# Kernel tuning notes

Measured on AMD Instinct MI355X. Metric: run time of the kernel, lower is better.

## Reference

```python
import jax, jax.numpy as jnp
import numpy as np

N = 512          # N_ROIs (nodes)
E = N * N        # number of edges
V = 6            # number of views (edge_attr dim)
DIMS = [(1, 36), (36, 24), (24, 5)]  # (in, out) per NNConv layer


def _nnconv(x, edge_attr, src, dst, We, be, root, bias, cin, cout):
    # edge MLP: Linear + ReLU -> per-edge weight matrix [E, cin, cout]
    w = jax.nn.relu(edge_attr @ We + be).reshape(-1, cin, cout)
    msg = jnp.einsum('ei,eio->eo', x[src], w)              # gather + per-edge matmul
    s = jax.ops.segment_sum(msg, dst, num_segments=N)      # scatter-sum
    cnt = jax.ops.segment_sum(jnp.ones((msg.shape[0], 1), x.dtype), dst, num_segments=N)
    agg = s / jnp.maximum(cnt, 1.0)                        # mean aggregation
    return agg + x @ root + bias                           # root weight + bias (PyG NNConv)


def setup_inputs() -> dict:
    key = jax.random.key(0)
    ks = jax.random.split(key, 16)
    x = jnp.ones((N, 1), jnp.float32)
    edge_attr = jax.random.uniform(ks[0], (E, V), jnp.float32)
    edge_index = jax.random.randint(ks[1], (2, E), 0, N, dtype=jnp.int32)
    inp = {'x': x, 'edge_attr': edge_attr, 'edge_index': edge_index}
    for l, (cin, cout) in enumerate(DIMS, start=1):
        k = jax.random.split(ks[1 + l], 4)
        inp[f'We{l}'] = jax.random.normal(k[0], (V, cin * cout), jnp.float32) / np.sqrt(V)
        inp[f'be{l}'] = jnp.zeros((cin * cout,), jnp.float32)
        inp[f'root{l}'] = jax.random.normal(k[1], (cin, cout), jnp.float32) / np.sqrt(cin)
        inp[f'b{l}'] = jnp.zeros((cout,), jnp.float32)
    return inp


def reference(x, edge_attr, edge_index,
              We1, be1, root1, b1,
              We2, be2, root2, b2,
              We3, be3, root3, b3):
    src, dst = edge_index[0], edge_index[1]
    h = jax.nn.relu(_nnconv(x, edge_attr, src, dst, We1, be1, root1, b1, *DIMS[0]))
    h = jax.nn.relu(_nnconv(h, edge_attr, src, dst, We2, be2, root2, b2, *DIMS[1]))
    h = jax.nn.relu(_nnconv(h, edge_attr, src, dst, We3, be3, root3, b3, *DIMS[2]))
    # pairwise CBT: sum_k |h_i,k - h_j,k|  ->  [N, N]
    cbt = jnp.sum(jnp.abs(h[:, None, :] - h[None, :, :]), axis=2)
    return cbt
```

## Files before the change

### kernel.cpp

```cpp
#include <hip/hip_runtime.h>
#include <hip/hip_bf16.h>
#include <hip/hip_fp16.h>

#define N_NODES 512
#define N_EDGES (512 * 512)
#define NBLK 256
#define EPB (N_EDGES / NBLK)
#define PADLEN 768

typedef __attribute__((ext_vector_type(8))) __bf16 bf16x8;
typedef __attribute__((ext_vector_type(16))) float f32x16;

static __device__ inline unsigned bf16rne(float f) {
    union { float f; unsigned u; } c;
    c.f = f;
    unsigned u = c.u;
    u += 0x7FFFu + ((u >> 16) & 1u);
    return u >> 16;
}
static __device__ inline float bf2f(unsigned h) {
    union { unsigned u; float f; } c;
    c.u = h << 16;
    return c.f;
}

__global__ __launch_bounds__(256) void count_kernel(const int* __restrict__ dst,
                                                    int* __restrict__ bcnt) {
    __shared__ int h[N_NODES];
    int tid = threadIdx.x;
    int b = blockIdx.x;
    h[tid] = 0;
    h[tid + 256] = 0;
    __syncthreads();
#pragma unroll
    for (int k = 0; k < EPB / 256; k++)
        atomicAdd(&h[dst[b * EPB + k * 256 + tid]], 1);
    __syncthreads();
    bcnt[b * N_NODES + tid] = h[tid];
    bcnt[b * N_NODES + tid + 256] = h[tid + 256];
}

__global__ __launch_bounds__(512) void scan_kernel(const int* __restrict__ bcnt,
                                                   int* __restrict__ offs,
                                                   int* __restrict__ base) {
    __shared__ int buf[N_NODES];
    int t = threadIdx.x;
    int sum = 0;
#pragma unroll 16
    for (int b = 0; b < NBLK; b++) sum += bcnt[b * N_NODES + t];
    buf[t] = sum;
    __syncthreads();
    for (int d = 1; d < N_NODES; d <<= 1) {
        int add = (t >= d) ? buf[t - d] : 0;
        __syncthreads();
        buf[t] += add;
        __syncthreads();
    }
    offs[t + 1] = buf[t];
    if (t == 0) offs[0] = 0;
    int run = buf[t] - sum;
#pragma unroll 16
    for (int b = 0; b < NBLK; b++) {
        base[b * N_NODES + t] = run;
        run += bcnt[b * N_NODES + t];
    }
}

__global__ __launch_bounds__(256) void scatter_kernel(const int* __restrict__ src,
                                                      const int* __restrict__ dst,
                                                      const float* __restrict__ ea,
                                                      const int* __restrict__ base,
                                                      const int* __restrict__ offs,
                                                      int4* __restrict__ edp,
                                                      int* __restrict__ srcp) {
    __shared__ int lcur[N_NODES];
    __shared__ int loff[N_NODES];
    int tid = threadIdx.x;
    int b = blockIdx.x;
    lcur[tid] = base[b * N_NODES + tid];
    lcur[tid + 256] = base[b * N_NODES + tid + 256];
    loff[tid] = offs[tid];
    loff[tid + 256] = offs[tid + 256];
    __syncthreads();
    const unsigned ONE = 0x3F80u;
#pragma unroll
    for (int k = 0; k < EPB / 256; k++) {
        int e = b * EPB + k * 256 + tid;
        const float* a = ea + (size_t)e * 6;
        unsigned e0 = bf16rne(a[0]), e1 = bf16rne(a[1]), e2 = bf16rne(a[2]);
        unsigned e3 = bf16rne(a[3]), e4 = bf16rne(a[4]), e5 = bf16rne(a[5]);
        int dv = dst[e], sv = src[e];
        int p = atomicAdd(&lcur[dv], 1);
        int rank = p - loff[dv];
        size_t pi = (size_t)dv * PADLEN + rank;
        int4 r0, r1;
        r0.x = (int)((e1 << 16) | e0);
        r0.y = (int)((e3 << 16) | e2);
        r0.z = (int)((e5 << 16) | e4);
        r0.w = (int)((e0 << 16) | ONE);
        r1.x = (int)((e2 << 16) | e1);
        r1.y = (int)((e4 << 16) | e3);
        r1.z = (int)((ONE << 16) | e5);
        r1.w = 0;
        edp[pi * 2] = r0;
        edp[pi * 2 + 1] = r1;
        srcp[pi] = sv;
    }
}

__global__ __launch_bounds__(256) void wprep_kernel(const float* __restrict__ We,
                                                    const float* __restrict__ be,
                                                    int Jr, int total,
                                                    int4* __restrict__ wtg) {
    int idx = blockIdx.x * 256 + threadIdx.x;
    if (idx >= total) return;
    int t = idx >> 6, lane = idx & 63, col = lane & 31, hi = lane >> 5;
    int j = t * 32 + col;
    unsigned h[8] = {0, 0, 0, 0, 0, 0, 0, 0};
    if (j < Jr) {
        unsigned wh[6];
        float wl[6];
        for (int v = 0; v < 6; v++) {
            float wv = We[v * Jr + j];
            wh[v] = bf16rne(wv);
            wl[v] = wv - bf2f(wh[v]);
        }
        float bev = be[j];
        unsigned bh = bf16rne(bev);
        float bl = bev - bf2f(bh);
        if (hi == 0) {
            for (int v = 0; v < 6; v++) h[v] = wh[v];
            h[6] = bh;
            h[7] = bf16rne(wl[0]);
        } else {
            for (int v = 1; v < 6; v++) h[v - 1] = bf16rne(wl[v]);
            h[5] = bf16rne(bl);
            h[6] = 0;
            h[7] = 0;
        }
    }
    int4 r;
    r.x = (int)((h[1] << 16) | h[0]);
    r.y = (int)((h[3] << 16) | h[2]);
    r.z = (int)((h[5] << 16) | h[4]);
    r.w = (int)((h[7] << 16) | h[6]);
    wtg[idx] = r;
}

template <int CIN, int COUT, int TILES, int SLOTS>
__global__ __launch_bounds__(512, 4) void nnconv_mfma(
    const float* __restrict__ hprev,
    const int4* __restrict__ edp,
    const int* __restrict__ srcp,
    const int* __restrict__ offs,
    const int4* __restrict__ wtg,
    const float* __restrict__ root,
    const float* __restrict__ bias,
    float* __restrict__ hout)
{
    __shared__ __half xs[N_NODES * CIN];
    __shared__ int4 wl[TILES * 64];
    __shared__ float lagg[COUT];

    const int tid = threadIdx.x;
    const int n = blockIdx.x;

    for (int k = tid; k < N_NODES * CIN; k += 512) xs[k] = __float2half(hprev[k]);
    for (int k = tid; k < TILES * 64; k += 512) wl[k] = wtg[k];
    if (tid < COUT) lagg[tid] = 0.f;
    __syncthreads();

    const int w = tid >> 6, lane = tid & 63;
    const int col = lane & 31, hi = lane >> 5;
    const char* xsp = (const char*)xs;
    const char* wlp = (const char*)wl + (hi * 32 + col) * 16;

    f32x16 zc;
#pragma unroll
    for (int q = 0; q < 16; q++) zc[q] = 0.f;

    float ao[SLOTS];
#pragma unroll
    for (int s = 0; s < SLOTS; s++) ao[s] = 0.f;

    const int nb = n * PADLEN + w * 96;

    for (int c = 0; c < 3; c++) {
        const int cb = nb + c * 32;
        bf16x8 af = *(const bf16x8*)((const char*)edp + (size_t)(cb + col) * 32 + hi * 16);
        int xb[16];
#pragma unroll
        for (int qq = 0; qq < 4; qq++) {
            int4 sv = *(const int4*)(srcp + cb + qq * 8 + hi * 4);
            xb[qq * 4 + 0] = sv.x * (CIN * 2);
            xb[qq * 4 + 1] = sv.y * (CIN * 2);
            xb[qq * 4 + 2] = sv.z * (CIN * 2);
            xb[qq * 4 + 3] = sv.w * (CIN * 2);
        }
        const char* wq = wlp;
        int jb = col;
#pragma unroll 1
        for (int tt = 0; tt < TILES / SLOTS; tt++) {
#pragma unroll
            for (int s = 0; s < SLOTS; s++) {
                bf16x8 bf = *(const bf16x8*)(wq + s * 1024);
                f32x16 ct = __builtin_amdgcn_mfma_f32_32x32x16_bf16(af, bf, zc, 0, 0, 0);
                int j = jb + s * 32;
                int i = j / COUT;
                if (i > CIN - 1) i = CIN - 1;
                int i2 = i * 2;
#pragma unroll
                for (int r = 0; r < 16; r++) {
                    float xv = __half2float(*(const __half*)(xsp + xb[r] + i2));
                    ao[s] = fmaf(fmaxf(ct[r], 0.f), xv, ao[s]);
                }
            }
            wq += SLOTS * 1024;
            jb += SLOTS * 32;
        }
    }

#pragma unroll
    for (int s = 0; s < SLOTS; s++) {
        int o = (s * 32 + col) % COUT;
        atomicAdd(&lagg[o], ao[s]);
    }
    __syncthreads();

    if (tid < COUT) {
        int cnt = offs[n + 1] - offs[n];
        float v = lagg[tid] / fmaxf((float)cnt, 1.f);
#pragma unroll
        for (int i = 0; i < CIN; i++)
            v = fmaf(hprev[n * CIN + i], root[i * COUT + tid], v);
        hout[n * COUT + tid] = fmaxf(v + bias[tid], 0.f);
    }
}

__global__ __launch_bounds__(256) void cbt_kernel(const float* __restrict__ h3,
                                                  float* __restrict__ out) {
    __shared__ float lh[N_NODES * 5];
    int tid = threadIdx.x;
    for (int idx = tid; idx < N_NODES * 5; idx += 256) lh[idx] = h3[idx];
    __syncthreads();
    int i = blockIdx.x;
    float hi[5];
#pragma unroll
    for (int k = 0; k < 5; k++) hi[k] = lh[i * 5 + k];
    for (int j = tid; j < N_NODES; j += 256) {
        float sacc = 0.f;
#pragma unroll
        for (int k = 0; k < 5; k++) sacc += fabsf(hi[k] - lh[j * 5 + k]);
        out[i * N_NODES + j] = sacc;
    }
}

extern "C" void kernel_launch(void* const* d_in, const int* in_sizes, int n_in,
                              void* d_out, int out_size, void* d_ws, size_t ws_size,
                              hipStream_t stream) {
    const float* x = (const float*)d_in[0];
    const float* edge_attr = (const float*)d_in[1];
    const int* edge_index = (const int*)d_in[2];
    const float* We1 = (const float*)d_in[3];
    const float* be1 = (const float*)d_in[4];
    const float* root1 = (const float*)d_in[5];
    const float* b1 = (const float*)d_in[6];
    const float* We2 = (const float*)d_in[7];
    const float* be2 = (const float*)d_in[8];
    const float* root2 = (const float*)d_in[9];
    const float* b2 = (const float*)d_in[10];
    const float* We3 = (const float*)d_in[11];
    const float* be3 = (const float*)d_in[12];
    const float* root3 = (const float*)d_in[13];
    const float* b3 = (const float*)d_in[14];

    const int E = N_EDGES;
    const int* src = edge_index;
    const int* dst = edge_index + E;

    char* ws = (char*)d_ws;
    int* offs = (int*)(ws + 0);
    int* bcnt = (int*)(ws + 4096);
    int* base = (int*)(ws + 528384);
    int4* edp = (int4*)(ws + 1052672);
    int* srcp = (int*)(ws + 13635584);
    int4* wtg1 = (int4*)(ws + 15208448);
    int4* wtg2 = (int4*)(ws + 15210496);
    int4* wtg3 = (int4*)(ws + 15238144);
    float* h1 = (float*)(ws + 15242240);
    float* h2 = (float*)(ws + 15315968);
    float* h3 = (float*)(ws + 15365120);

    hipMemsetAsync(edp, 0, (size_t)N_NODES * PADLEN * 32 + (size_t)N_NODES * PADLEN * 4, stream);

    count_kernel<<<NBLK, 256, 0, stream>>>(dst, bcnt);
    scan_kernel<<<1, 512, 0, stream>>>(bcnt, offs, base);
    scatter_kernel<<<NBLK, 256, 0, stream>>>(src, dst, edge_attr, base, offs, edp, srcp);

    wprep_kernel<<<1, 256, 0, stream>>>(We1, be1, 36, 2 * 64, wtg1);
    wprep_kernel<<<7, 256, 0, stream>>>(We2, be2, 864, 27 * 64, wtg2);
    wprep_kernel<<<1, 256, 0, stream>>>(We3, be3, 120, 4 * 64, wtg3);

    nnconv_mfma<1, 36, 2, 2><<<N_NODES, 512, 0, stream>>>(x, edp, srcp, offs, wtg1, root1, b1, h1);
    nnconv_mfma<36, 24, 27, 3><<<N_NODES, 512, 0, stream>>>(h1, edp, srcp, offs, wtg2, root2, b2, h2);
    nnconv_mfma<24, 5, 4, 4><<<N_NODES, 512, 0, stream>>>(h2, edp, srcp, offs, wtg3, root3, b3, h3);

    cbt_kernel<<<N_NODES, 256, 0, stream>>>(h3, (float*)d_out);
}
```

Measured before the change: 220.2 us.

## Swap MFMA operand roles and pad weight layout to per-input-channel tiles

Swaps the MFMA operands so edges lie along the column dimension and weight outputs along the rows. Weights are padded so each tile row maps to a single input channel, which lets each lane hold its source node's features in registers. Loaded once per edge chunk from a padded half-precision copy emitted by the previous layer, they replace per-row LDS gathers and the full LDS staging of hprev. Reduction moves to cross-lane shuffles before the LDS atomics. In exchange, padding adds more MFMA tiles (36 vs 27 for layer 2) and more accumulator registers.

```diff
diff --git a/kernel.cpp b/kernel.cpp
--- a/kernel.cpp
+++ b/kernel.cpp
@@ -22,6 +22,9 @@
     union { unsigned u; float f; } c;
     c.u = h << 16;
     return c.f;
+}
+static __device__ __forceinline__ int i4c(const int4& v, int c) {
+    return c == 0 ? v.x : (c == 1 ? v.y : (c == 2 ? v.z : v.w));
 }
 
 __global__ __launch_bounds__(256) void count_kernel(const int* __restrict__ dst,
@@ -42,9 +45,12 @@
 
 __global__ __launch_bounds__(512) void scan_kernel(const int* __restrict__ bcnt,
                                                    int* __restrict__ offs,
-                                                   int* __restrict__ base) {
+                                                   int* __restrict__ base,
+                                                   const float* __restrict__ x,
+                                                   __half* __restrict__ xh) {
     __shared__ int buf[N_NODES];
     int t = threadIdx.x;
+    xh[t] = __float2half(x[t]);
     int sum = 0;
 #pragma unroll 16
     for (int b = 0; b < NBLK; b++) sum += bcnt[b * N_NODES + t];
@@ -110,14 +116,17 @@
 
 __global__ __launch_bounds__(256) void wprep_kernel(const float* __restrict__ We,
                                                     const float* __restrict__ be,
-                                                    int Jr, int total,
-                                                    int4* __restrict__ wtg) {
+                                                    int cin, int cout, int osl,
+                                                    int total, int4* __restrict__ wtg) {
     int idx = blockIdx.x * 256 + threadIdx.x;
     if (idx >= total) return;
     int t = idx >> 6, lane = idx & 63, col = lane & 31, hi = lane >> 5;
-    int j = t * 32 + col;
+    int jpp = t * 32 + col;
+    int i = jpp / osl, o = jpp % osl;
+    int Jr = cin * cout;
     unsigned h[8] = {0, 0, 0, 0, 0, 0, 0, 0};
-    if (j < Jr) {
+    if (o < cout && i < cin) {
+        int j = i * cout + o;
         unsigned wh[6];
         float wl[6];
         for (int v = 0; v < 6; v++) {
@@ -135,8 +144,6 @@
         } else {
             for (int v = 1; v < 6; v++) h[v - 1] = bf16rne(wl[v]);
             h[5] = bf16rne(bl);
-            h[6] = 0;
-            h[7] = 0;
         }
     }
     int4 r;
@@ -147,83 +154,92 @@
     wtg[idx] = r;
 }
 
-template <int CIN, int COUT, int TILES, int SLOTS>
+template <int CIN, int COUT, int TILES, int OSL, int PIN, int POUT>
 __global__ __launch_bounds__(512, 4) void nnconv_mfma(
     const float* __restrict__ hprev,
+    const __half* __restrict__ hhin,
     const int4* __restrict__ edp,
     const int* __restrict__ srcp,
     const int* __restrict__ offs,
     const int4* __restrict__ wtg,
     const float* __restrict__ root,
     const float* __restrict__ bias,
-    float* __restrict__ hout)
+    float* __restrict__ hout,
+    __half* __restrict__ hhout)
 {
-    __shared__ __half xs[N_NODES * CIN];
+    constexpr int TPI = (OSL + 31) / 32;
+    constexpr int NACC = TPI * 16;
     __shared__ int4 wl[TILES * 64];
     __shared__ float lagg[COUT];
 
     const int tid = threadIdx.x;
     const int n = blockIdx.x;
-
-    for (int k = tid; k < N_NODES * CIN; k += 512) xs[k] = __float2half(hprev[k]);
     for (int k = tid; k < TILES * 64; k += 512) wl[k] = wtg[k];
     if (tid < COUT) lagg[tid] = 0.f;
     __syncthreads();
 
     const int w = tid >> 6, lane = tid & 63;
     const int col = lane & 31, hi = lane >> 5;
-    const char* xsp = (const char*)xs;
     const char* wlp = (const char*)wl + (hi * 32 + col) * 16;
 
     f32x16 zc;
 #pragma unroll
     for (int q = 0; q < 16; q++) zc[q] = 0.f;
 
-    float ao[SLOTS];
-#pragma unroll
-    for (int s = 0; s < SLOTS; s++) ao[s] = 0.f;
+    float acc[NACC];
+#pragma unroll
+    for (int a = 0; a < NACC; a++) acc[a] = 0.f;
 
     const int nb = n * PADLEN + w * 96;
 
+#pragma unroll 1
     for (int c = 0; c < 3; c++) {
         const int cb = nb + c * 32;
-        bf16x8 af = *(const bf16x8*)((const char*)edp + (size_t)(cb + col) * 32 + hi * 16);
-        int xb[16];
-#pragma unroll
-        for (int qq = 0; qq < 4; qq++) {
-            int4 sv = *(const int4*)(srcp + cb + qq * 8 + hi * 4);
-            xb[qq * 4 + 0] = sv.x * (CIN * 2);
-            xb[qq * 4 + 1] = sv.y * (CIN * 2);
-            xb[qq * 4 + 2] = sv.z * (CIN * 2);
-            xb[qq * 4 + 3] = sv.w * (CIN * 2);
-        }
-        const char* wq = wlp;
-        int jb = col;
-#pragma unroll 1
-        for (int tt = 0; tt < TILES / SLOTS; tt++) {
-#pragma unroll
-            for (int s = 0; s < SLOTS; s++) {
-                bf16x8 bf = *(const bf16x8*)(wq + s * 1024);
-                f32x16 ct = __builtin_amdgcn_mfma_f32_32x32x16_bf16(af, bf, zc, 0, 0, 0);
-                int j = jb + s * 32;
-                int i = j / COUT;
-                if (i > CIN - 1) i = CIN - 1;
-                int i2 = i * 2;
-#pragma unroll
-                for (int r = 0; r < 16; r++) {
-                    float xv = __half2float(*(const __half*)(xsp + xb[r] + i2));
-                    ao[s] = fmaf(fmaxf(ct[r], 0.f), xv, ao[s]);
-                }
+        bf16x8 bfrag = *(const bf16x8*)((const char*)edp + (size_t)(cb + col) * 32 + hi * 16);
+        int sv = srcp[cb + col] & 511;
+        float xf[CIN];
+        if constexpr (CIN == 1) {
+            xf[0] = __half2float(hhin[sv]);
+        } else {
+            constexpr int NV4 = PIN / 8;
+            const int4* hp = (const int4*)(hhin + sv * PIN);
+            int4 xr[NV4];
+#pragma unroll
+            for (int q = 0; q < NV4; q++) xr[q] = hp[q];
+#pragma unroll
+            for (int i = 0; i < CIN; i++) {
+                union { int d; __half2 h; } u;
+                u.d = i4c(xr[i >> 3], (i >> 1) & 3);
+                xf[i] = __half2float((i & 1) ? u.h.y : u.h.x);
             }
-            wq += SLOTS * 1024;
-            jb += SLOTS * 32;
-        }
-    }
-
-#pragma unroll
-    for (int s = 0; s < SLOTS; s++) {
-        int o = (s * 32 + col) % COUT;
-        atomicAdd(&lagg[o], ao[s]);
+        }
+#pragma unroll
+        for (int t = 0; t < TILES; t++) {
+            bf16x8 afrag = *(const bf16x8*)(wlp + t * 1024);
+            f32x16 ct = __builtin_amdgcn_mfma_f32_32x32x16_bf16(afrag, bfrag, zc, 0, 0, 0);
+#pragma unroll
+            for (int r = 0; r < 16; r++) {
+                const int jlb = (r & 3) + 8 * (r >> 2);
+                const int i = (t * 32 + jlb) / OSL;
+                const int a = (t % TPI) * 16 + r;
+                acc[a] = fmaf(fmaxf(ct[r], 0.f), xf[i], acc[a]);
+            }
+        }
+    }
+
+#pragma unroll
+    for (int a = 0; a < NACC; a++) {
+        const int tm = a >> 4, r = a & 15;
+        const int jlb = (r & 3) + 8 * (r >> 2);
+        const int ob = (tm * 32 + jlb) % OSL;
+        float v = acc[a];
+        v += __shfl_xor(v, 1);
+        v += __shfl_xor(v, 2);
+        v += __shfl_xor(v, 4);
+        v += __shfl_xor(v, 8);
+        v += __shfl_xor(v, 16);
+        int o = ob + 4 * hi;
+        if ((lane & 31) == 0 && o < COUT) atomicAdd(&lagg[o], v);
     }
     __syncthreads();
 
@@ -233,7 +249,13 @@
 #pragma unroll
         for (int i = 0; i < CIN; i++)
             v = fmaf(hprev[n * CIN + i], root[i * COUT + tid], v);
-        hout[n * COUT + tid] = fmaxf(v + bias[tid], 0.f);
+        v = fmaxf(v + bias[tid], 0.f);
+        hout[n * COUT + tid] = v;
+        if constexpr (POUT > 0) hhout[n * POUT + tid] = __float2half(v);
+    } else {
+        if constexpr (POUT > 0) {
+            if (tid < POUT) hhout[n * POUT + tid] = __float2half(0.f);
+        }
     }
 }
 
@@ -286,24 +308,30 @@
     int* srcp = (int*)(ws + 13635584);
     int4* wtg1 = (int4*)(ws + 15208448);
     int4* wtg2 = (int4*)(ws + 15210496);
-    int4* wtg3 = (int4*)(ws + 15238144);
-    float* h1 = (float*)(ws + 15242240);
-    float* h2 = (float*)(ws + 15315968);
-    float* h3 = (float*)(ws + 15365120);
+    int4* wtg3 = (int4*)(ws + 15247360);
+    float* h1 = (float*)(ws + 15253504);
+    float* h2 = (float*)(ws + 15327232);
+    float* h3 = (float*)(ws + 15376384);
+    __half* xh = (__half*)(ws + 15386624);
+    __half* hh1 = (__half*)(ws + 15387648);
+    __half* hh2 = (__half*)(ws + 15428608);
 
     hipMemsetAsync(edp, 0, (size_t)N_NODES * PADLEN * 32 + (size_t)N_NODES * PADLEN * 4, stream);
 
     count_kernel<<<NBLK, 256, 0, stream>>>(dst, bcnt);
-    scan_kernel<<<1, 512, 0, stream>>>(bcnt, offs, base);
+    scan_kernel<<<1, 512, 0, stream>>>(bcnt, offs, base, x, xh);
     scatter_kernel<<<NBLK, 256, 0, stream>>>(src, dst, edge_attr, base, offs, edp, srcp);
 
-    wprep_kernel<<<1, 256, 0, stream>>>(We1, be1, 36, 2 * 64, wtg1);
-    wprep_kernel<<<7, 256, 0, stream>>>(We2, be2, 864, 27 * 64, wtg2);
-    wprep_kernel<<<1, 256, 0, stream>>>(We3, be3, 120, 4 * 64, wtg3);
-
-    nnconv_mfma<1, 36, 2, 2><<<N_NODES, 512, 0, stream>>>(x, edp, srcp, offs, wtg1, root1, b1, h1);
-    nnconv_mfma<36, 24, 27, 3><<<N_NODES, 512, 0, stream>>>(h1, edp, srcp, offs, wtg2, root2, b2, h2);
-    nnconv_mfma<24, 5, 4, 4><<<N_NODES, 512, 0, stream>>>(h2, edp, srcp, offs, wtg3, root3, b3, h3);
+    wprep_kernel<<<1, 256, 0, stream>>>(We1, be1, 1, 36, 64, 2 * 64, wtg1);
+    wprep_kernel<<<9, 256, 0, stream>>>(We2, be2, 36, 24, 32, 36 * 64, wtg2);
+    wprep_kernel<<<2, 256, 0, stream>>>(We3, be3, 24, 5, 8, 6 * 64, wtg3);
+
+    nnconv_mfma<1, 36, 2, 64, 1, 40><<<N_NODES, 512, 0, stream>>>(
+        x, xh, edp, srcp, offs, wtg1, root1, b1, h1, hh1);
+    nnconv_mfma<36, 24, 36, 32, 40, 24><<<N_NODES, 512, 0, stream>>>(
+        h1, hh1, edp, srcp, offs, wtg2, root2, b2, h2, hh2);
+    nnconv_mfma<24, 5, 6, 8, 24, 0><<<N_NODES, 512, 0, stream>>>(
+        h2, hh2, edp, srcp, offs, wtg3, root3, b3, h3, (__half*)nullptr);
 
     cbt_kernel<<<N_NODES, 256, 0, stream>>>(h3, (float*)d_out);
 }
```

New measurement: 717.7 us. 226% more time.
